# Performance work log

Measured on AMD Instinct MI355X. Metric: run time of the kernel, lower is better.

The kernel has to match this reference:

```python
import jax, jax.numpy as jnp
import numpy as np

N = 50000
E = 800000
IN_DIM = 256
HID = 64
HEADS = 6
OUT_DIM = 32
NEG_SLOPE = 0.2


def gat_conv(x, src, dst, W, att_src, att_dst, bias, heads, ch, n_nodes):
    """PyG GATConv (eval mode): lin proj, per-edge LeakyReLU attention,
    segment softmax over destination neighborhoods, scatter-add aggregate.
    src/dst already include self-loops. Returns [n_nodes, heads, ch]."""
    h = (x @ W).reshape(n_nodes, heads, ch)            # [N,H,C]
    a_src = jnp.sum(h * att_src, axis=-1)              # [N,H]
    a_dst = jnp.sum(h * att_dst, axis=-1)              # [N,H]
    e = jax.nn.leaky_relu(a_src[src] + a_dst[dst], NEG_SLOPE)   # [E,H]
    m = jax.ops.segment_max(e, dst, num_segments=n_nodes)       # [N,H]
    ex = jnp.exp(e - m[dst])                                    # [E,H]
    denom = jax.ops.segment_sum(ex, dst, num_segments=n_nodes)  # [N,H]
    alpha = ex / denom[dst]                                     # [E,H]
    out = jax.ops.segment_sum(h[src] * alpha[:, :, None], dst, num_segments=n_nodes)
    return out + bias.reshape(1, heads, ch)


def setup_inputs() -> dict:
    key = jax.random.key(0)
    ks = jax.random.split(key, 10)
    x = jax.random.normal(ks[0], (N, IN_DIM), dtype=jnp.float32)
    edge_index = jax.random.randint(ks[1], (2, E), 0, N, dtype=jnp.int64)
    s1 = 1.0 / np.sqrt(IN_DIM)
    W1 = jax.random.normal(ks[2], (IN_DIM, HEADS * HID), dtype=jnp.float32) * s1
    att_src1 = jax.random.normal(ks[3], (1, HEADS, HID), dtype=jnp.float32) * 0.1
    att_dst1 = jax.random.normal(ks[4], (1, HEADS, HID), dtype=jnp.float32) * 0.1
    b1 = jnp.zeros((HEADS * HID,), dtype=jnp.float32)
    s2 = 1.0 / np.sqrt(HEADS * HID)
    W2 = jax.random.normal(ks[5], (HEADS * HID, OUT_DIM), dtype=jnp.float32) * s2
    att_src2 = jax.random.normal(ks[6], (1, 1, OUT_DIM), dtype=jnp.float32) * 0.1
    att_dst2 = jax.random.normal(ks[7], (1, 1, OUT_DIM), dtype=jnp.float32) * 0.1
    b2 = jnp.zeros((OUT_DIM,), dtype=jnp.float32)
    return {"x": x, "edge_index": edge_index, "W1": W1, "att_src1": att_src1,
            "att_dst1": att_dst1, "b1": b1, "W2": W2, "att_src2": att_src2,
            "att_dst2": att_dst2, "b2": b2}


def reference(x, edge_index, W1, att_src1, att_dst1, b1, W2, att_src2, att_dst2, b2):
    # PyG GATConv default add_self_loops=True
    loops = jnp.arange(N, dtype=edge_index.dtype)
    src = jnp.concatenate([edge_index[0], loops])
    dst = jnp.concatenate([edge_index[1], loops])
    h1 = gat_conv(x, src, dst, W1, att_src1, att_dst1, b1, HEADS, HID, N)
    h1 = jax.nn.relu(h1.reshape(N, HEADS * HID))  # concat=True, then ReLU; dropout = identity (eval)
    h2 = gat_conv(h1, src, dst, W2, att_src2, att_dst2, b2, 1, OUT_DIM, N)
    return h2.reshape(N, OUT_DIM)  # concat=False with 1 head == mean == squeeze
```

## Files before the change

### kernel.cpp

```cpp
#include <hip/hip_runtime.h>
#include <hip/hip_bf16.h>

#define NN 50000
#define EE 800000
#define IN_DIM 256
#define HID 64
#define HEADS 6
#define D1 384
#define OUT_DIM 32
#define NEG_SLOPE 0.2f
#define CAP 128
#define NBLK 196

typedef unsigned int uint32;
typedef unsigned short ushort_t;
typedef short short8 __attribute__((ext_vector_type(8)));
typedef float f32x4 __attribute__((ext_vector_type(4)));
typedef float f32x2 __attribute__((ext_vector_type(2)));
typedef ushort_t ushort8 __attribute__((ext_vector_type(8)));

__device__ __forceinline__ ushort_t f2bf(float f) {
    uint32 u = __builtin_bit_cast(uint32, f);
    u += 0x7fffu + ((u >> 16) & 1u);
    return (ushort_t)(u >> 16);
}
__device__ __forceinline__ float bf2f(ushort_t s) {
    uint32 u = ((uint32)s) << 16;
    return __builtin_bit_cast(float, u);
}
__device__ __forceinline__ float lo16(uint32 d) { return __builtin_bit_cast(float, d << 16); }
__device__ __forceinline__ float hi16(uint32 d) { return __builtin_bit_cast(float, d & 0xffff0000u); }


__global__ __launch_bounds__(256) void prep_kernel(const float* __restrict__ W1,
                                                   ushort_t* __restrict__ W1Tb,
                                                   const float* __restrict__ W2,
                                                   ushort_t* __restrict__ W2Tb,
                                                   int* __restrict__ deg) {
    int bx = blockIdx.x;
    if (bx < 96) {
        __shared__ float tile[32][33];
        int tx = threadIdx.x & 31, ty = threadIdx.x >> 5;
        int n0 = (bx % 12) * 32;
        int k0 = (bx / 12) * 32;
#pragma unroll
        for (int i = 0; i < 4; ++i)
            tile[ty + i * 8][tx] = W1[(k0 + ty + i * 8) * D1 + n0 + tx];
        __syncthreads();
#pragma unroll
        for (int i = 0; i < 4; ++i)
            W1Tb[(n0 + ty + i * 8) * IN_DIM + k0 + tx] = f2bf(tile[tx][ty + i * 8]);
    } else if (bx < 144) {
        int idx = (bx - 96) * 256 + threadIdx.x;
        if (idx < D1 * OUT_DIM) {
            int k = idx >> 5, n = idx & 31;
            W2Tb[n * D1 + k] = f2bf(W2[idx]);
        }
    } else {
        int i = (bx - 144) * 256 + threadIdx.x;
        if (i < NN) deg[i] = 0;
    }
}


__global__ void hist_kernel(const int* __restrict__ dst, int* __restrict__ deg) {
    int i = blockIdx.x * 256 + threadIdx.x;
    if (i < EE) atomicAdd(&deg[dst[i]], 1);
}

__global__ __launch_bounds__(256) void scan1_kernel(const int* __restrict__ deg,
                                                    int* __restrict__ blockSums) {
    int t = threadIdx.x;
    int i = blockIdx.x * 256 + t;
    int v = (i < NN) ? (deg[i] + 1) : 0;
#pragma unroll
    for (int o = 32; o; o >>= 1) v += __shfl_xor(v, o);
    __shared__ int ws[4];
    if ((t & 63) == 0) ws[t >> 6] = v;
    __syncthreads();
    if (t == 0) blockSums[blockIdx.x] = ws[0] + ws[1] + ws[2] + ws[3];
}

__global__ __launch_bounds__(256) void scan2_kernel(const int* __restrict__ blockSums,
                                                    int* __restrict__ blockPrefix,
                                                    int* __restrict__ offsets) {
    int t = threadIdx.x;
    int lane = t & 63, w = t >> 6;
    int v = (t < NBLK) ? blockSums[t] : 0;
    int x = v;
#pragma unroll
    for (int o = 1; o < 64; o <<= 1) {
        int y = __shfl_up(x, o);
        if (lane >= o) x += y;
    }
    __shared__ int ws[4];
    if (lane == 63) ws[w] = x;
    __syncthreads();
    int wpre = 0;
#pragma unroll
    for (int k = 0; k < 4; ++k) if (k < w) wpre += ws[k];
    int incl = x + wpre;
    if (t < NBLK) blockPrefix[t] = incl - v;
    if (t == NBLK - 1) offsets[NN] = incl;
}

__global__ __launch_bounds__(256) void scan3_kernel(const int* __restrict__ deg,
                                                    const int* __restrict__ blockPrefix,
                                                    int* __restrict__ offsets,
                                                    int* __restrict__ cursor) {
    int t = threadIdx.x;
    int i = blockIdx.x * 256 + t;
    int lane = t & 63, w = t >> 6;
    int v = (i < NN) ? (deg[i] + 1) : 0;
    int x = v;
#pragma unroll
    for (int o = 1; o < 64; o <<= 1) {
        int y = __shfl_up(x, o);
        if (lane >= o) x += y;
    }
    __shared__ int ws[4];
    if (lane == 63) ws[w] = x;
    __syncthreads();
    int wpre = 0;
#pragma unroll
    for (int k = 0; k < 4; ++k) if (k < w) wpre += ws[k];
    int excl = x + wpre - v + blockPrefix[blockIdx.x];
    if (i < NN) { offsets[i] = excl; cursor[i] = excl; }
}

__global__ void scatter_kernel(const int* __restrict__ src, const int* __restrict__ dst,
                               int* __restrict__ cursor, int* __restrict__ srcIdx) {
    int i = blockIdx.x * 256 + threadIdx.x;
    if (i >= EE + NN) return;
    int s, d;
    if (i < EE) { s = src[i]; d = dst[i]; }
    else        { s = i - EE; d = s; }
    int pos = atomicAdd(&cursor[d], 1);
    srcIdx[pos] = s;
}


#define G1_BM 128
#define G1_BK 64

__global__ __launch_bounds__(512) void gemm1_kernel(const float* __restrict__ A,
                                                    const ushort_t* __restrict__ Bt,
                                                    const float* __restrict__ att_src,
                                                    const float* __restrict__ att_dst,
                                                    ushort_t* __restrict__ Cb,
                                                    float* __restrict__ a_src1,
                                                    float* __restrict__ a_dst1) {
    __shared__ __align__(16) ushort_t As[G1_BM][G1_BK];
    __shared__ __align__(16) ushort_t Bs[D1][G1_BK];
    __shared__ float redS[G1_BM][8];
    __shared__ float redD[G1_BM][8];
    int t = threadIdx.x;
    int m0 = blockIdx.x * G1_BM;
    int wid = t >> 6, lane = t & 63;
    int rg = wid >> 2, cg = wid & 3;
    int lrow = lane & 15, lk = lane >> 4;
    f32x4 acc[4][6] = {};
    for (int k0 = 0; k0 < IN_DIM; k0 += G1_BK) {
        {
            int r = t >> 3, c = t & 7;
#pragma unroll
            for (int p = 0; p < 2; ++p) {
                int row = p * 64 + r;
                int gr = m0 + row;
                float4 v0 = make_float4(0.f, 0.f, 0.f, 0.f), v1 = v0;
                if (gr < NN) {
                    const float* g = &A[(size_t)gr * IN_DIM + k0 + c * 8];
                    v0 = *reinterpret_cast<const float4*>(g);
                    v1 = *reinterpret_cast<const float4*>(g + 4);
                }
                ushort8 u;
                u[0] = f2bf(v0.x); u[1] = f2bf(v0.y); u[2] = f2bf(v0.z); u[3] = f2bf(v0.w);
                u[4] = f2bf(v1.x); u[5] = f2bf(v1.y); u[6] = f2bf(v1.z); u[7] = f2bf(v1.w);
                *reinterpret_cast<ushort8*>(&As[row][(c ^ (row & 7)) * 8]) = u;
            }
        }
        {
            int r = t >> 3, c = t & 7;
#pragma unroll
            for (int p = 0; p < 6; ++p) {
                int row = p * 64 + r;
                ushort8 u = *reinterpret_cast<const ushort8*>(&Bt[row * IN_DIM + k0 + c * 8]);
                *reinterpret_cast<ushort8*>(&Bs[row][(c ^ (row & 7)) * 8]) = u;
            }
        }
        __syncthreads();
#pragma unroll
        for (int kk = 0; kk < G1_BK; kk += 32) {
            int ckb = (kk >> 3) + lk;
            short8 af[4];
#pragma unroll
            for (int fm = 0; fm < 4; ++fm) {
                int m = rg * 64 + fm * 16 + lrow;
                af[fm] = *reinterpret_cast<const short8*>(&As[m][(ckb ^ (m & 7)) * 8]);
            }
#pragma unroll
            for (int fn = 0; fn < 6; ++fn) {
                int n = cg * 96 + fn * 16 + lrow;
                short8 bfv = *reinterpret_cast<const short8*>(&Bs[n][(ckb ^ (n & 7)) * 8]);
#pragma unroll
                for (int fm = 0; fm < 4; ++fm)
                    acc[fm][fn] = __builtin_amdgcn_mfma_f32_16x16x32_bf16(af[fm], bfv, acc[fm][fn], 0, 0, 0);
            }
        }
        __syncthreads();
    }
    float atS[6], atD[6];
#pragma unroll
    for (int fn = 0; fn < 6; ++fn) {
        int col = cg * 96 + fn * 16 + lrow;
        atS[fn] = att_src[col];
        atD[fn] = att_dst[col];
    }
    int split = (cg & 1) ? 2 : 4;
#pragma unroll
    for (int fm = 0; fm < 4; ++fm) {
#pragma unroll
        for (int r = 0; r < 4; ++r) {
            int rowl = rg * 64 + fm * 16 + lk * 4 + r;
            int row = m0 + rowl;
            float vsA = 0.f, vsB = 0.f, vdA = 0.f, vdB = 0.f;
#pragma unroll
            for (int fn = 0; fn < 6; ++fn) {
                float v = acc[fm][fn][r];
                if (fn < split) { vsA += v * atS[fn]; vdA += v * atD[fn]; }
                else            { vsB += v * atS[fn]; vdB += v * atD[fn]; }
            }
#pragma unroll
            for (int o = 8; o; o >>= 1) {
                vsA += __shfl_xor(vsA, o); vsB += __shfl_xor(vsB, o);
                vdA += __shfl_xor(vdA, o); vdB += __shfl_xor(vdB, o);
            }
            if (lrow == 0) {
                redS[rowl][cg * 2 + 0] = vsA; redS[rowl][cg * 2 + 1] = vsB;
                redD[rowl][cg * 2 + 0] = vdA; redD[rowl][cg * 2 + 1] = vdB;
            }
            if (row < NN) {
#pragma unroll
                for (int fn = 0; fn < 6; ++fn) {
                    int col = cg * 96 + fn * 16 + lrow;
                    Cb[(size_t)row * D1 + col] = f2bf(acc[fm][fn][r]);
                }
            }
        }
    }
    __syncthreads();
    if (t < G1_BM) {
        int row = m0 + t;
        if (row < NN) {
            float s0 = redS[t][0], s1 = redS[t][1] + redS[t][2], s2 = redS[t][3];
            float s3 = redS[t][4], s4 = redS[t][5] + redS[t][6], s5 = redS[t][7];
            float d0 = redD[t][0], d1 = redD[t][1] + redD[t][2], d2 = redD[t][3];
            float d3 = redD[t][4], d4 = redD[t][5] + redD[t][6], d5 = redD[t][7];
            float* ps = &a_src1[(size_t)row * HEADS];
            float* pd = &a_dst1[(size_t)row * HEADS];
            ps[0] = s0; ps[1] = s1; ps[2] = s2; ps[3] = s3; ps[4] = s4; ps[5] = s5;
            pd[0] = d0; pd[1] = d1; pd[2] = d2; pd[3] = d3; pd[4] = d4; pd[5] = d5;
        }
    }
}


__global__ __launch_bounds__(256, 4) void agg1_kernel(const uint32* __restrict__ H1d,
                                                      const float* __restrict__ a_src,
                                                      const float* __restrict__ a_dst,
                                                      const int* __restrict__ offsets,
                                                      const int* __restrict__ srcIdx,
                                                      const float* __restrict__ b1,
                                                      uint32* __restrict__ out1d) {
    __shared__ float pl[4][HEADS][CAP + 1];
    __shared__ int   sl[4][CAP];
    int w = threadIdx.x >> 6, lane = threadIdx.x & 63;
    int hb = lane >> 5;
    int n = blockIdx.x * 4 + w;
    const float2* asv = (const float2*)a_src;
    float ad[HEADS];
#pragma unroll
    for (int h = 0; h < HEADS; ++h) ad[h] = a_dst[n * HEADS + h];
    float ldn[HEADS] = {0.f, 0.f, 0.f, 0.f, 0.f, 0.f};
    float acc[6] = {0.f, 0.f, 0.f, 0.f, 0.f, 0.f};
    int beg = offsets[n], end = offsets[n + 1];
    for (int cbeg = beg; cbeg < end; cbeg += CAP) {
        int L = end - cbeg; if (L > CAP) L = CAP;
        for (int tI = lane; tI < L; tI += 64) {
            int s = srcIdx[cbeg + tI];
            sl[w][tI] = s;
            float2 e0 = asv[s * 3 + 0];
            float2 e1 = asv[s * 3 + 1];
            float2 e2 = asv[s * 3 + 2];
            float ev[6] = {e0.x, e0.y, e1.x, e1.y, e2.x, e2.y};
#pragma unroll
            for (int h = 0; h < HEADS; ++h) {
                float e = ev[h] + ad[h];
                e = e > 0.f ? e : NEG_SLOPE * e;
                float p = __expf(e);
                pl[w][h][tI] = p;
                ldn[h] += p;
            }
        }
        int j = 0;
        for (; j + 4 <= L; j += 4) {
            int s0 = sl[w][j], s1 = sl[w][j + 1], s2 = sl[w][j + 2], s3 = sl[w][j + 3];
            const uint32* h0 = H1d + (size_t)s0 * 192 + lane;
            const uint32* h1 = H1d + (size_t)s1 * 192 + lane;
            const uint32* h2 = H1d + (size_t)s2 * 192 + lane;
            const uint32* h3 = H1d + (size_t)s3 * 192 + lane;
            uint32 a0 = h0[0], a1 = h0[64], a2 = h0[128];
            uint32 b0 = h1[0], b1v_ = h1[64], b2 = h1[128];
            uint32 c0 = h2[0], c1 = h2[64], c2 = h2[128];
            uint32 d0 = h3[0], d1 = h3[64], d2 = h3[128];
            float p00 = pl[w][hb][j],     p01 = pl[w][2 + hb][j],     p02 = pl[w][4 + hb][j];
            float p10 = pl[w][hb][j + 1], p11 = pl[w][2 + hb][j + 1], p12 = pl[w][4 + hb][j + 1];
            float p20 = pl[w][hb][j + 2], p21 = pl[w][2 + hb][j + 2], p22 = pl[w][4 + hb][j + 2];
            float p30 = pl[w][hb][j + 3], p31 = pl[w][2 + hb][j + 3], p32 = pl[w][4 + hb][j + 3];
            acc[0] += p00 * lo16(a0); acc[1] += p00 * hi16(a0);
            acc[2] += p01 * lo16(a1); acc[3] += p01 * hi16(a1);
            acc[4] += p02 * lo16(a2); acc[5] += p02 * hi16(a2);
            acc[0] += p10 * lo16(b0); acc[1] += p10 * hi16(b0);
            acc[2] += p11 * lo16(b1v_); acc[3] += p11 * hi16(b1v_);
            acc[4] += p12 * lo16(b2); acc[5] += p12 * hi16(b2);
            acc[0] += p20 * lo16(c0); acc[1] += p20 * hi16(c0);
            acc[2] += p21 * lo16(c1); acc[3] += p21 * hi16(c1);
            acc[4] += p22 * lo16(c2); acc[5] += p22 * hi16(c2);
            acc[0] += p30 * lo16(d0); acc[1] += p30 * hi16(d0);
            acc[2] += p31 * lo16(d1); acc[3] += p31 * hi16(d1);
            acc[4] += p32 * lo16(d2); acc[5] += p32 * hi16(d2);
        }
        for (; j < L; ++j) {
            int s0 = sl[w][j];
            const uint32* h0 = H1d + (size_t)s0 * 192 + lane;
            uint32 x0 = h0[0], x1 = h0[64], x2 = h0[128];
            float p0 = pl[w][hb][j], p1 = pl[w][2 + hb][j], p2 = pl[w][4 + hb][j];
            acc[0] += p0 * lo16(x0); acc[1] += p0 * hi16(x0);
            acc[2] += p1 * lo16(x1); acc[3] += p1 * hi16(x1);
            acc[4] += p2 * lo16(x2); acc[5] += p2 * hi16(x2);
        }
    }
#pragma unroll
    for (int h = 0; h < HEADS; ++h) {
#pragma unroll
        for (int o = 32; o; o >>= 1) ldn[h] += __shfl_xor(ldn[h], o);
    }
    float dsel[3];
#pragma unroll
    for (int k = 0; k < 3; ++k) dsel[k] = hb ? ldn[2 * k + 1] : ldn[2 * k];
    const float2* b1v = (const float2*)b1;
#pragma unroll
    for (int k = 0; k < 3; ++k) {
        float2 bb = b1v[k * 64 + lane];
        float v0 = fmaxf(acc[2 * k]     / dsel[k] + bb.x, 0.f);
        float v1 = fmaxf(acc[2 * k + 1] / dsel[k] + bb.y, 0.f);
        uint32 pk = (uint32)f2bf(v0) | ((uint32)f2bf(v1) << 16);
        __builtin_nontemporal_store(pk, &out1d[(size_t)n * 192 + k * 64 + lane]);
    }
}


#define G2_ROWS 256

__global__ __launch_bounds__(256) void gemm2_kernel(const ushort_t* __restrict__ Xb,
                                                    const ushort_t* __restrict__ W2Tb,
                                                    const float* __restrict__ att_src2,
                                                    const float* __restrict__ att_dst2,
                                                    ushort_t* __restrict__ H2b,
                                                    float* __restrict__ a_src2,
                                                    float* __restrict__ a_dst2) {
    __shared__ __align__(16) ushort_t Ws[OUT_DIM][D1];
    __shared__ __align__(16) ushort_t Xs[G2_ROWS][64];
    int t = threadIdx.x;
    int wid = t >> 6, lane = t & 63;
    int lrow = lane & 15, lk = lane >> 4;
    int m0 = blockIdx.x * G2_ROWS;
#pragma unroll
    for (int p = 0; p < 6; ++p) {
        int chunk = p * 256 + t;
        int nr = chunk / 48, c = chunk % 48;
        ushort8 u = *reinterpret_cast<const ushort8*>(&W2Tb[nr * D1 + c * 8]);
        int span = c >> 3, cc = c & 7;
        *reinterpret_cast<ushort8*>(&Ws[nr][(cc ^ (nr & 7)) * 8 + span * 64]) = u;
    }
    f32x4 acc[4][2] = {};
    for (int kc = 0; kc < 6; ++kc) {
        int k0 = kc * 64;
        {
            int r = t >> 3, c = t & 7;
#pragma unroll
            for (int p = 0; p < 8; ++p) {
                int row = p * 32 + r;
                int gr = m0 + row;
                ushort8 u = {0, 0, 0, 0, 0, 0, 0, 0};
                if (gr < NN) u = *reinterpret_cast<const ushort8*>(&Xb[(size_t)gr * D1 + k0 + c * 8]);
                *reinterpret_cast<ushort8*>(&Xs[row][(c ^ (row & 7)) * 8]) = u;
            }
        }
        __syncthreads();
#pragma unroll
        for (int kk = 0; kk < 64; kk += 32) {
            int ckb = (kk >> 3) + lk;
            short8 af[4];
#pragma unroll
            for (int fm = 0; fm < 4; ++fm) {
                int mm = wid * 64 + fm * 16 + lrow;
                af[fm] = *reinterpret_cast<const short8*>(&Xs[mm][(ckb ^ (mm & 7)) * 8]);
            }
#pragma unroll
            for (int fn = 0; fn < 2; ++fn) {
                int nn2 = fn * 16 + lrow;
                short8 bfv = *reinterpret_cast<const short8*>(&Ws[nn2][(ckb ^ (nn2 & 7)) * 8 + kc * 64]);
#pragma unroll
                for (int fm = 0; fm < 4; ++fm)
                    acc[fm][fn] = __builtin_amdgcn_mfma_f32_16x16x32_bf16(af[fm], bfv, acc[fm][fn], 0, 0, 0);
            }
        }
        __syncthreads();
    }
    float as2a = att_src2[lrow], as2b = att_src2[16 + lrow];
    float ad2a = att_dst2[lrow], ad2b = att_dst2[16 + lrow];
#pragma unroll
    for (int fm = 0; fm < 4; ++fm) {
#pragma unroll
        for (int r = 0; r < 4; ++r) {
            int row = m0 + wid * 64 + fm * 16 + lk * 4 + r;
            float h0 = acc[fm][0][r], h1 = acc[fm][1][r];
            float vs = h0 * as2a + h1 * as2b;
            float vd = h0 * ad2a + h1 * ad2b;
#pragma unroll
            for (int o = 8; o; o >>= 1) {
                vs += __shfl_xor(vs, o);
                vd += __shfl_xor(vd, o);
            }
            if (row < NN) {
                H2b[(size_t)row * OUT_DIM + lrow]      = f2bf(h0);
                H2b[(size_t)row * OUT_DIM + 16 + lrow] = f2bf(h1);
                if (lrow == 0) { a_src2[row] = vs; a_dst2[row] = vd; }
            }
        }
    }
}


__global__ __launch_bounds__(256, 4) void agg2_kernel(const ushort_t* __restrict__ H2b,
                                                      const float* __restrict__ a_src,
                                                      const float* __restrict__ a_dst,
                                                      const int* __restrict__ offsets,
                                                      const int* __restrict__ srcIdx,
                                                      const float* __restrict__ b2,
                                                      float* __restrict__ out) {
    __shared__ float pl[4][CAP];
    __shared__ int   sl[4][CAP];
    int w = threadIdx.x >> 6, lane = threadIdx.x & 63;
    int n = blockIdx.x * 4 + w;
    int q = lane & 15, par = lane >> 4;
    const uint32* H2d = (const uint32*)H2b;
    float ad = a_dst[n];
    float ldn = 0.f, ax = 0.f, ay = 0.f;
    int beg = offsets[n], end = offsets[n + 1];
    for (int cbeg = beg; cbeg < end; cbeg += CAP) {
        int L = end - cbeg; if (L > CAP) L = CAP;
        for (int tI = lane; tI < L; tI += 64) {
            int s = srcIdx[cbeg + tI];
            sl[w][tI] = s;
            float e = a_src[s] + ad;
            e = e > 0.f ? e : NEG_SLOPE * e;
            float p = __expf(e);
            pl[w][tI] = p;
            ldn += p;
        }
        int j = 0;
        for (; j + 8 <= L; j += 8) {
            int s0 = sl[w][j + par], s1 = sl[w][j + 4 + par];
            float p0 = pl[w][j + par], p1 = pl[w][j + 4 + par];
            uint32 d0 = H2d[(size_t)s0 * 16 + q];
            uint32 d1 = H2d[(size_t)s1 * 16 + q];
            ax += p0 * lo16(d0) + p1 * lo16(d1);
            ay += p0 * hi16(d0) + p1 * hi16(d1);
        }
        for (; j < L; j += 4) {
            int jj = j + par;
            if (jj < L) {
                int s = sl[w][jj];
                float p = pl[w][jj];
                uint32 d = H2d[(size_t)s * 16 + q];
                ax += p * lo16(d);
                ay += p * hi16(d);
            }
        }
    }
#pragma unroll
    for (int o = 32; o; o >>= 1) ldn += __shfl_xor(ldn, o);
    ax += __shfl_xor(ax, 16); ax += __shfl_xor(ax, 32);
    ay += __shfl_xor(ay, 16); ay += __shfl_xor(ay, 32);
    if (lane < 16) {
        float2 bb = ((const float2*)b2)[q];
        f32x2 o;
        o[0] = ax / ldn + bb.x;
        o[1] = ay / ldn + bb.y;
        __builtin_nontemporal_store(o, (f32x2*)&out[(size_t)n * 32 + q * 2]);
    }
}


static inline size_t align256(size_t x) { return (x + 255) & ~size_t(255); }

extern "C" void kernel_launch(void* const* d_in, const int* in_sizes, int n_in,
                              void* d_out, int out_size, void* d_ws, size_t ws_size,
                              hipStream_t stream) {
    const float* x        = (const float*)d_in[0];
    const int*   ei       = (const int*)d_in[1];
    const float* W1       = (const float*)d_in[2];
    const float* att_src1 = (const float*)d_in[3];
    const float* att_dst1 = (const float*)d_in[4];
    const float* b1       = (const float*)d_in[5];
    const float* W2       = (const float*)d_in[6];
    const float* att_src2 = (const float*)d_in[7];
    const float* att_dst2 = (const float*)d_in[8];
    const float* b2       = (const float*)d_in[9];
    float* out = (float*)d_out;

    const int* e_src = ei;
    const int* e_dst = ei + EE;

    char* p = (char*)d_ws;
    ushort_t* H1b   = (ushort_t*)p; p += align256(sizeof(ushort_t) * (size_t)NN * D1);
    ushort_t* OUT1b = (ushort_t*)p; p += align256(sizeof(ushort_t) * (size_t)NN * D1);
    ushort_t* H2b   = (ushort_t*)p; p += align256(sizeof(ushort_t) * (size_t)NN * OUT_DIM);
    ushort_t* W1Tb  = (ushort_t*)p; p += align256(sizeof(ushort_t) * D1 * IN_DIM);
    ushort_t* W2Tb  = (ushort_t*)p; p += align256(sizeof(ushort_t) * D1 * OUT_DIM);
    float* AS1  = (float*)p; p += align256(sizeof(float) * NN * HEADS);
    float* AD1  = (float*)p; p += align256(sizeof(float) * NN * HEADS);
    float* AS2  = (float*)p; p += align256(sizeof(float) * NN);
    float* AD2  = (float*)p; p += align256(sizeof(float) * NN);
    int*   DEG  = (int*)p;   p += align256(sizeof(int) * NN);
    int*   OFF  = (int*)p;   p += align256(sizeof(int) * (NN + 1));
    int*   CUR  = (int*)p;   p += align256(sizeof(int) * NN);
    int*   BSUM = (int*)p;   p += align256(sizeof(int) * NBLK);
    int*   BPRE = (int*)p;   p += align256(sizeof(int) * NBLK);
    int*   SIDX = (int*)p;   p += align256(sizeof(int) * (EE + NN));

    prep_kernel<<<340, 256, 0, stream>>>(W1, W1Tb, W2, W2Tb, DEG);
    hist_kernel<<<(EE + 255) / 256, 256, 0, stream>>>(e_dst, DEG);
    scan1_kernel<<<NBLK, 256, 0, stream>>>(DEG, BSUM);
    scan2_kernel<<<1, 256, 0, stream>>>(BSUM, BPRE, OFF);
    scan3_kernel<<<NBLK, 256, 0, stream>>>(DEG, BPRE, OFF, CUR);
    scatter_kernel<<<(EE + NN + 255) / 256, 256, 0, stream>>>(e_src, e_dst, CUR, SIDX);

    gemm1_kernel<<<(NN + G1_BM - 1) / G1_BM, 512, 0, stream>>>(x, W1Tb, att_src1, att_dst1, H1b, AS1, AD1);
    agg1_kernel<<<NN / 4, 256, 0, stream>>>((const uint32*)H1b, AS1, AD1, OFF, SIDX, b1, (uint32*)OUT1b);

    gemm2_kernel<<<(NN + G2_ROWS - 1) / G2_ROWS, 256, 0, stream>>>(OUT1b, W2Tb, att_src2, att_dst2, H2b, AS2, AD2);
    agg2_kernel<<<NN / 4, 256, 0, stream>>>(H2b, AS2, AD2, OFF, SIDX, b2, out);
}
```

Baseline: 313.3 us.

## Pre-swizzle W1 for direct global-to-LDS loads and simplify agg2 edge loop

The prep kernel now writes the transposed bf16 W1 in a pre-swizzled, k-tiled layout, so the GEMM1 kernel can fill its B tile with global_load_lds DMA instead of loading into registers and storing to LDS. Separately, agg2 drops its shared-memory staging of source indices and weights: each lane group now computes its own edge weights inline and gathers directly, with the denominator rescaled by 1/16 to undo the replicated sums. This removes LDS traffic and a staging pass, but makes 16 lanes recompute the same exp per edge and removes the 2-way unrolled gather.

```diff
diff --git a/kernel.cpp b/kernel.cpp
--- a/kernel.cpp
+++ b/kernel.cpp
@@ -31,9 +31,15 @@
 __device__ __forceinline__ float lo16(uint32 d) { return __builtin_bit_cast(float, d << 16); }
 __device__ __forceinline__ float hi16(uint32 d) { return __builtin_bit_cast(float, d & 0xffff0000u); }
 
+__device__ __forceinline__ void gload_lds16(const void* g, void* l) {
+    __builtin_amdgcn_global_load_lds(
+        (const __attribute__((address_space(1))) unsigned int*)g,
+        (__attribute__((address_space(3))) unsigned int*)l, 16, 0, 0);
+}
+
 
 __global__ __launch_bounds__(256) void prep_kernel(const float* __restrict__ W1,
-                                                   ushort_t* __restrict__ W1Tb,
+                                                   ushort_t* __restrict__ W1TbSwz,
                                                    const float* __restrict__ W2,
                                                    ushort_t* __restrict__ W2Tb,
                                                    int* __restrict__ deg) {
@@ -48,8 +54,14 @@
             tile[ty + i * 8][tx] = W1[(k0 + ty + i * 8) * D1 + n0 + tx];
         __syncthreads();
 #pragma unroll
-        for (int i = 0; i < 4; ++i)
-            W1Tb[(n0 + ty + i * 8) * IN_DIM + k0 + tx] = f2bf(tile[tx][ty + i * 8]);
+        for (int i = 0; i < 4; ++i) {
+            int n = n0 + ty + i * 8;
+            int k = k0 + tx;
+            int t = k >> 6;
+            int cc = (k >> 3) & 7;
+            int L = n * 8 + (cc ^ (n & 7));
+            W1TbSwz[t * 24576 + L * 8 + (k & 7)] = f2bf(tile[tx][ty + i * 8]);
+        }
     } else if (bx < 144) {
         int idx = (bx - 96) * 256 + threadIdx.x;
         if (idx < D1 * OUT_DIM) {
@@ -162,6 +174,14 @@
     f32x4 acc[4][6] = {};
     for (int k0 = 0; k0 < IN_DIM; k0 += G1_BK) {
         {
+            const ushort_t* bsrc = Bt + (size_t)k0 * 384;
+#pragma unroll
+            for (int i = 0; i < 6; ++i) {
+                int blk = i * 8 + wid;
+                gload_lds16(bsrc + blk * 512 + lane * 8, &Bs[0][0] + blk * 512);
+            }
+        }
+        {
             int r = t >> 3, c = t & 7;
 #pragma unroll
             for (int p = 0; p < 2; ++p) {
@@ -177,15 +197,6 @@
                 u[0] = f2bf(v0.x); u[1] = f2bf(v0.y); u[2] = f2bf(v0.z); u[3] = f2bf(v0.w);
                 u[4] = f2bf(v1.x); u[5] = f2bf(v1.y); u[6] = f2bf(v1.z); u[7] = f2bf(v1.w);
                 *reinterpret_cast<ushort8*>(&As[row][(c ^ (row & 7)) * 8]) = u;
-            }
-        }
-        {
-            int r = t >> 3, c = t & 7;
-#pragma unroll
-            for (int p = 0; p < 6; ++p) {
-                int row = p * 64 + r;
-                ushort8 u = *reinterpret_cast<const ushort8*>(&Bt[row * IN_DIM + k0 + c * 8]);
-                *reinterpret_cast<ushort8*>(&Bs[row][(c ^ (row & 7)) * 8]) = u;
             }
         }
         __syncthreads();
@@ -443,15 +454,13 @@
 }
 
 
-__global__ __launch_bounds__(256, 4) void agg2_kernel(const ushort_t* __restrict__ H2b,
-                                                      const float* __restrict__ a_src,
-                                                      const float* __restrict__ a_dst,
-                                                      const int* __restrict__ offsets,
-                                                      const int* __restrict__ srcIdx,
-                                                      const float* __restrict__ b2,
-                                                      float* __restrict__ out) {
-    __shared__ float pl[4][CAP];
-    __shared__ int   sl[4][CAP];
+__global__ __launch_bounds__(256) void agg2_kernel(const ushort_t* __restrict__ H2b,
+                                                   const float* __restrict__ a_src,
+                                                   const float* __restrict__ a_dst,
+                                                   const int* __restrict__ offsets,
+                                                   const int* __restrict__ srcIdx,
+                                                   const float* __restrict__ b2,
+                                                   float* __restrict__ out) {
     int w = threadIdx.x >> 6, lane = threadIdx.x & 63;
     int n = blockIdx.x * 4 + w;
     int q = lane & 15, par = lane >> 4;
@@ -459,39 +468,19 @@
     float ad = a_dst[n];
     float ldn = 0.f, ax = 0.f, ay = 0.f;
     int beg = offsets[n], end = offsets[n + 1];
-    for (int cbeg = beg; cbeg < end; cbeg += CAP) {
-        int L = end - cbeg; if (L > CAP) L = CAP;
-        for (int tI = lane; tI < L; tI += 64) {
-            int s = srcIdx[cbeg + tI];
-            sl[w][tI] = s;
-            float e = a_src[s] + ad;
-            e = e > 0.f ? e : NEG_SLOPE * e;
-            float p = __expf(e);
-            pl[w][tI] = p;
-            ldn += p;
-        }
-        int j = 0;
-        for (; j + 8 <= L; j += 8) {
-            int s0 = sl[w][j + par], s1 = sl[w][j + 4 + par];
-            float p0 = pl[w][j + par], p1 = pl[w][j + 4 + par];
-            uint32 d0 = H2d[(size_t)s0 * 16 + q];
-            uint32 d1 = H2d[(size_t)s1 * 16 + q];
-            ax += p0 * lo16(d0) + p1 * lo16(d1);
-            ay += p0 * hi16(d0) + p1 * hi16(d1);
-        }
-        for (; j < L; j += 4) {
-            int jj = j + par;
-            if (jj < L) {
-                int s = sl[w][jj];
-                float p = pl[w][jj];
-                uint32 d = H2d[(size_t)s * 16 + q];
-                ax += p * lo16(d);
-                ay += p * hi16(d);
-            }
-        }
+    for (int j = beg + par; j < end; j += 4) {
+        int s = srcIdx[j];
+        float e = a_src[s] + ad;
+        e = e > 0.f ? e : NEG_SLOPE * e;
+        float p = __expf(e);
+        uint32 d = H2d[(size_t)s * 16 + q];
+        ldn += p;
+        ax += p * lo16(d);
+        ay += p * hi16(d);
     }
 #pragma unroll
     for (int o = 32; o; o >>= 1) ldn += __shfl_xor(ldn, o);
+    ldn *= 0.0625f;
     ax += __shfl_xor(ax, 16); ax += __shfl_xor(ax, 32);
     ay += __shfl_xor(ay, 16); ay += __shfl_xor(ay, 32);
     if (lane < 16) {
```

Result: no change. 317.2 us (+1.2%).
